# Optimization experiments

Hardware: AMD Instinct MI355X
Metric: run time of the kernel (lower is better)

Reference implementation:

```python
import jax, jax.numpy as jnp
import numpy as np

# NCHW 3x3 conv, padding=1. BatchNorm (inference affine) is folded into conv weight/bias,
# which is mathematically identical to Conv->BN(eval) in the original.
def conv3(x, w, b, stride):
    y = jax.lax.conv_general_dilated(x, w, (stride, stride), [(1, 1), (1, 1)],
                                     dimension_numbers=('NCHW', 'OIHW', 'NCHW'))
    return y + b[None, :, None, None]

def lin1(x, w, b):  # 1x1 conv as channel matmul; w: [out, in]
    return jnp.einsum('oc,bchw->bohw', w, x) + b[None, :, None, None]

def setup_inputs():
    key = jax.random.key(0)
    ks = list(jax.random.split(key, 32))
    C, M = 32, 32  # cv_hypo_num, mid_dim (kq_dim == mid_dim since mid_dim <= 128)
    B, H, W = 1, 256, 512
    w3 = lambda k, o, i: jax.random.normal(k, (o, i, 3, 3), jnp.float32) * 0.05
    w1 = lambda k, o, i: jax.random.normal(k, (o, i), jnp.float32) * 0.05
    bv = lambda k, o: jax.random.normal(k, (o,), jnp.float32) * 0.01
    inp = {
        'mono_pseudo_cost': jax.random.normal(ks[0], (B, C, H, W), jnp.float32),
        'cost_volume': jax.random.normal(ks[1], (B, C, H, W), jnp.float32),
        # mono_expand / multi_expand: two stride-2 conv(+folded BN)+ReLU blocks each
        'me_w1': w3(ks[2], M, C), 'me_b1': bv(ks[3], M),
        'me_w2': w3(ks[4], M, C), 'me_b2': bv(ks[5], M),
        'xe_w1': w3(ks[6], M, C), 'xe_b1': bv(ks[7], M),
        'xe_w2': w3(ks[8], M, C), 'xe_b2': bv(ks[9], M),
        # 1x1 q/k/v projections for both branches
        'mq_w': w1(ks[10], M, M), 'mq_b': bv(ks[11], M),
        'mk_w': w1(ks[12], M, M), 'mk_b': bv(ks[13], M),
        'mv_w': w1(ks[14], M, M), 'mv_b': bv(ks[15], M),
        'xq_w': w1(ks[16], M, M), 'xq_b': bv(ks[17], M),
        'xk_w': w1(ks[18], M, M), 'xk_b': bv(ks[19], M),
        'xv_w': w1(ks[20], M, M), 'xv_b': bv(ks[21], M),
        # residual branches
        'mr_w1': w3(ks[22], M, C), 'mr_b1': bv(ks[23], M),
        'mr_w2': w3(ks[24], M, C), 'mr_b2': bv(ks[25], M),
        'xr_w': w1(ks[26], M, C), 'xr_b': bv(ks[27], M),
        'gamma': jnp.full((1,), 0.5, jnp.float32),  # nonzero so attention path is live
    }
    return inp

def reference(mono_pseudo_cost, cost_volume,
              me_w1, me_b1, me_w2, me_b2,
              xe_w1, xe_b1, xe_w2, xe_b2,
              mq_w, mq_b, mk_w, mk_b, mv_w, mv_b,
              xq_w, xq_b, xk_w, xk_b, xv_w, xv_b,
              mr_w1, mr_b1, mr_w2, mr_b2,
              xr_w, xr_b, gamma):
    relu = jax.nn.relu
    init_h, init_w = cost_volume.shape[2], cost_volume.shape[3]
    M = me_w1.shape[0]
    # feature extractors (stride-2 x2): [B,32,256,512] -> [B,32,64,128]
    mono_feat = relu(conv3(relu(conv3(mono_pseudo_cost, me_w1, me_b1, 2)), me_w2, me_b2, 2))
    multi_feat = relu(conv3(relu(conv3(cost_volume, xe_w1, xe_b1, 2)), xe_w2, xe_b2, 2))
    b, c, h, w = multi_feat.shape
    hw = h * w
    # q/k/v as [B, C, hw]
    mono_q = lin1(mono_feat, mq_w, mq_b).reshape(b, -1, hw)
    mono_k = lin1(mono_feat, mk_w, mk_b).reshape(b, -1, hw)
    mono_v = lin1(mono_feat, mv_w, mv_b).reshape(b, -1, hw)
    multi_q = lin1(multi_feat, xq_w, xq_b).reshape(b, -1, hw)
    multi_k = lin1(multi_feat, xk_w, xk_b).reshape(b, -1, hw)
    multi_v = lin1(multi_feat, xv_w, xv_b).reshape(b, -1, hw)
    # full [B, hw, hw] attention, no 1/sqrt(d) scaling (as in original)
    mono_atten = jax.nn.softmax(jnp.einsum('bci,bcj->bij', mono_q, mono_k), axis=-1)
    multi_atten = jax.nn.softmax(jnp.einsum('bci,bcj->bij', multi_q, multi_k), axis=-1)
    # cross application: mono values weighted by multi attention and vice versa
    mono_out = jnp.einsum('bcj,bij->bci', mono_v, multi_atten).reshape(b, M, h, w)
    multi_out = jnp.einsum('bcj,bij->bci', multi_v, mono_atten).reshape(b, M, h, w)
    fused = jnp.concatenate([multi_out, mono_out], axis=1)
    # nearest-neighbor upsample back to input size (integer factor 4)
    fused = jnp.repeat(jnp.repeat(fused, init_h // h, axis=2), init_w // w, axis=3)
    # residual branches
    mono_residual = relu(conv3(relu(conv3(mono_pseudo_cost, mr_w1, mr_b1, 1)), mr_w2, mr_b2, 1))
    multi_residual = relu(lin1(cost_volume, xr_w, xr_b))
    fused = jnp.concatenate([mono_residual, multi_residual], axis=1) + gamma * fused
    return fused
```

## Files before the change

### kernel.cpp

```cpp
#include <hip/hip_runtime.h>


using bf16x8 = __attribute__((ext_vector_type(8))) short;
using f32x4  = __attribute__((ext_vector_type(4))) float;
using f32x16 = __attribute__((ext_vector_type(16))) float;
typedef unsigned short u16;
typedef unsigned int   u32;

__device__ __forceinline__ u16 f2bf(float f) {
  u32 u = __builtin_bit_cast(u32, f);
  u = (u + 0x7fffu + ((u >> 16) & 1u)) >> 16;
  return (u16)u;
}
__device__ __forceinline__ float bf2f(u16 v) {
  u32 u = ((u32)v) << 16;
  return __builtin_bit_cast(float, u);
}
__device__ __forceinline__ u32 pktr(float lo, float hi) {
  return __builtin_amdgcn_perm(__builtin_bit_cast(u32, hi),
                               __builtin_bit_cast(u32, lo), 0x07060302u);
}
__device__ __forceinline__ f32x4 mfma16(bf16x8 a, bf16x8 b, f32x4 c) {
  return __builtin_amdgcn_mfma_f32_16x16x32_bf16(a, b, c, 0, 0, 0);
}
__device__ __forceinline__ f32x16 mfma32(bf16x8 a, bf16x8 b, f32x16 c) {
  return __builtin_amdgcn_mfma_f32_32x32x16_bf16(a, b, c, 0, 0, 0);
}
__device__ __forceinline__ f32x16 zero16() {
  f32x16 z = {0,0,0,0,0,0,0,0,0,0,0,0,0,0,0,0};
  return z;
}
__device__ __forceinline__ void store4bf(u16* dst, f32x4 v) {
  u32 lo = (u32)f2bf(v[0]) | ((u32)f2bf(v[1]) << 16);
  u32 hi = (u32)f2bf(v[2]) | ((u32)f2bf(v[3]) << 16);
  *(uint2*)dst = make_uint2(lo, hi);
}
__device__ __forceinline__ float sum16(const float* e) {
  float s0 = e[0] + e[1], s1 = e[2] + e[3], s2 = e[4] + e[5], s3 = e[6] + e[7];
  float s4 = e[8] + e[9], s5 = e[10] + e[11], s6 = e[12] + e[13], s7 = e[14] + e[15];
  float a = s0 + s1, b = s2 + s3, c = s4 + s5, d = s6 + s7;
  return (a + b) + (c + d);
}

struct WPtrs { const float* p[13]; };

__global__ void k_pre(WPtrs wp, u16* __restrict__ wConv, u16* __restrict__ w1x1,
                      const float* __restrict__ mono, const float* __restrict__ cv,
                      u16* __restrict__ monoT, u16* __restrict__ cvT,
                      u16* __restrict__ m1T, u16* __restrict__ x1T, u16* __restrict__ r1T) {
  int bx = blockIdx.x, t = threadIdx.x;
  if (bx < 13) {
    if (bx < 6) {
      const float* s = wp.p[bx];
      u16* d = wConv + bx * 9216;
      for (int i = t; i < 9216; i += 256) {
        int tap = i >> 10, co = (i >> 5) & 31, ci = i & 31;
        d[i] = f2bf(s[co * 288 + ci * 9 + tap]);
      }
    } else {
      const float* s = wp.p[bx];
      u16* d = w1x1 + (bx - 6) * 1024;
      for (int i = t; i < 1024; i += 256) d[i] = f2bf(s[i]);
    }
    return;
  }
  if (bx < 138) {
    int zb = bx - 13;
    int buf = zb % 5, blk = zb / 5;
    u16* b; int Hp, Wp;
    switch (buf) {
      case 0: b = monoT; Hp = 258; Wp = 514; break;
      case 1: b = cvT;   Hp = 258; Wp = 514; break;
      case 2: b = m1T;   Hp = 130; Wp = 258; break;
      case 3: b = x1T;   Hp = 130; Wp = 258; break;
      default: b = r1T;  Hp = 258; Wp = 514; break;
    }
    int id = blk * 256 + t;
    int cell = id >> 2, c8 = (id & 3) << 3;
    if (cell >= 2 * (Hp + Wp)) return;
    int r, c;
    if (cell < Wp)              { r = 0;                 c = cell; }
    else if (cell < 2 * Wp)     { r = Hp - 1;            c = cell - Wp; }
    else if (cell < 2 * Wp + Hp){ r = cell - 2 * Wp;     c = 0; }
    else                        { r = cell - 2 * Wp - Hp; c = Wp - 1; }
    bf16x8 z = {0, 0, 0, 0, 0, 0, 0, 0};
    *(bf16x8*)&b[(r * Wp + c) * 32 + c8] = z;
    return;
  }
  int idx = bx - 138;
  int xb = idx & 7, y = (idx >> 3) & 255, z = idx >> 11;
  const float* src = z ? cv : mono;
  u16* dst = z ? cvT : monoT;
  int x0 = xb << 6;
  __shared__ u16 tile[64][40];
  int ci = t >> 3, kx = (t & 7) << 3;
  const float* sp = src + ci * 131072 + y * 512 + x0 + kx;
  float4 a = *(const float4*)sp;
  float4 bb = *(const float4*)(sp + 4);
  tile[kx + 0][ci] = f2bf(a.x); tile[kx + 1][ci] = f2bf(a.y);
  tile[kx + 2][ci] = f2bf(a.z); tile[kx + 3][ci] = f2bf(a.w);
  tile[kx + 4][ci] = f2bf(bb.x); tile[kx + 5][ci] = f2bf(bb.y);
  tile[kx + 6][ci] = f2bf(bb.z); tile[kx + 7][ci] = f2bf(bb.w);
  __syncthreads();
  int x = t >> 2, c8 = (t & 3) << 3;
  bf16x8 v = *(bf16x8*)&tile[x][c8];
  *(bf16x8*)(dst + ((y + 1) * 514 + (x0 + x + 1)) * 32 + c8) = v;
}

__device__ __forceinline__ void conv3x3_body(int bxl, int tid,
    const u16* __restrict__ inT, int Wp, const u16* __restrict__ w9,
    const float* __restrict__ bias, u16* __restrict__ out, int outPitch,
    int outOff, int Ho, int tprShift, int stride) {
  int wid = (bxl * 256 + tid) >> 6;
  int lane = tid & 63, ln = lane & 15, q = lane >> 4;
  int y = wid >> tprShift;
  int x0 = (wid & ((1 << tprShift) - 1)) << 4;
  if (y >= Ho) return;
  f32x4 acc0 = *(const f32x4*)(bias + q * 4);
  f32x4 acc1 = *(const f32x4*)(bias + 16 + q * 4);
  const u16* ib = inT + (stride * y * Wp + stride * (x0 + ln)) * 32 + q * 8;
  const u16* wb = w9 + ln * 32 + q * 8;
#pragma unroll
  for (int dy = 0; dy < 3; ++dy)
#pragma unroll
    for (int dx = 0; dx < 3; ++dx) {
      int tap = dy * 3 + dx;
      bf16x8 bf = *(const bf16x8*)(ib + (dy * Wp + dx) * 32);
      acc0 = mfma16(*(const bf16x8*)(wb + tap * 1024), bf, acc0);
      acc1 = mfma16(*(const bf16x8*)(wb + tap * 1024 + 512), bf, acc1);
    }
#pragma unroll
  for (int r = 0; r < 4; ++r) { acc0[r] = fmaxf(acc0[r], 0.f); acc1[r] = fmaxf(acc1[r], 0.f); }
  u16* ob = out + (outOff + y * outPitch + x0 + ln) * 32;
  store4bf(ob + q * 4, acc0);
  store4bf(ob + 16 + q * 4, acc1);
}

__global__ void k_convs(const u16* __restrict__ monoT, const u16* __restrict__ cvT,
                        const u16* __restrict__ wConv,
                        const float* me_b1, const float* xe_b1, const float* mr_b1,
                        u16* __restrict__ m1T, u16* __restrict__ x1T, u16* __restrict__ r1T) {
  int bx = blockIdx.x;
  if (bx < 512)
    conv3x3_body(bx, threadIdx.x, monoT, 514, wConv + 0 * 9216, me_b1, m1T, 258, 259, 128, 4, 2);
  else if (bx < 1024)
    conv3x3_body(bx - 512, threadIdx.x, cvT, 514, wConv + 2 * 9216, xe_b1, x1T, 258, 259, 128, 4, 2);
  else
    conv3x3_body(bx - 1024, threadIdx.x, monoT, 514, wConv + 4 * 9216, mr_b1, r1T, 514, 515, 256, 5, 1);
}

__global__ void k_feat(const u16* __restrict__ m1T, const u16* __restrict__ x1T,
                       const u16* __restrict__ wConv,
                       const float* me_b2, const float* xe_b2,
                       u16* __restrict__ featM, u16* __restrict__ featX) {
  int bx = blockIdx.x;
  if (bx < 128)
    conv3x3_body(bx, threadIdx.x, m1T, 258, wConv + 1 * 9216, me_b2, featM, 128, 0, 64, 3, 2);
  else
    conv3x3_body(bx - 128, threadIdx.x, x1T, 258, wConv + 3 * 9216, xe_b2, featX, 128, 0, 64, 3, 2);
}

__global__ void k_proj(const u16* __restrict__ featM, const u16* __restrict__ featX,
                       const u16* __restrict__ w1x1,
                       const float* mq_b, const float* mk_b, const float* mv_b,
                       const float* xq_b, const float* xk_b, const float* xv_b,
                       u16* Qm, u16* Km, u16* Vm, u16* Qx, u16* Kx, u16* Vx) {
  int which = blockIdx.y;
  const u16* feat = (which < 3) ? featM : featX;
  const float* bias; u16* dst; float scale = 1.f; int cmode = 0;
  switch (which) {
    case 0: bias = mq_b; dst = Qm; scale = 1.4426950408889634f; break;
    case 1: bias = mk_b; dst = Km; break;
    case 2: bias = mv_b; dst = Vm; cmode = 1; break;
    case 3: bias = xq_b; dst = Qx; scale = 1.4426950408889634f; break;
    case 4: bias = xk_b; dst = Kx; break;
    default: bias = xv_b; dst = Vx; cmode = 1; break;
  }
  const u16* w = w1x1 + which * 1024;
  int wave = threadIdx.x >> 6, lane = threadIdx.x & 63, ln = lane & 15, q = lane >> 4;
  int p0 = (blockIdx.x * 4 + wave) << 4;
  bf16x8 bf = *(const bf16x8*)(feat + (p0 + ln) * 32 + q * 8);
  bf16x8 a0 = *(const bf16x8*)(w + ln * 32 + q * 8);
  bf16x8 a1 = *(const bf16x8*)(w + (16 + ln) * 32 + q * 8);
  f32x4 acc0 = *(const f32x4*)(bias + q * 4);
  f32x4 acc1 = *(const f32x4*)(bias + 16 + q * 4);
  acc0 = mfma16(a0, bf, acc0);
  acc1 = mfma16(a1, bf, acc1);
#pragma unroll
  for (int r = 0; r < 4; ++r) { acc0[r] *= scale; acc1[r] *= scale; }
  if (!cmode) {
    store4bf(dst + (p0 + ln) * 32 + q * 4, acc0);
    store4bf(dst + (p0 + ln) * 32 + 16 + q * 4, acc1);
  } else {
    int p = p0 + ln;
    int jl = p & 63, jb = p & ~63;
    int pj = jb + (jl >> 5) * 32 + ((jl >> 4) & 1) * 16 + ((jl >> 2) & 1) * 8
           + ((jl >> 3) & 1) * 4 + (jl & 3);
#pragma unroll
    for (int r = 0; r < 4; ++r) {
      dst[(q * 4 + r) * 8192 + pj] = f2bf(acc0[r]);
      dst[(16 + q * 4 + r) * 8192 + pj] = f2bf(acc1[r]);
    }
  }
}

__global__ void __launch_bounds__(256, 4) k_attention(
    const u16* __restrict__ Qm, const u16* __restrict__ Km, const u16* __restrict__ Vm,
    const u16* __restrict__ Qx, const u16* __restrict__ Kx, const u16* __restrict__ Vx,
    u16* __restrict__ Opart, float* __restrict__ lpart) {
  const u16 *Qp, *Kp, *Vp;
  int att = blockIdx.z;
  if (att == 0) { Qp = Qm; Kp = Km; Vp = Vx; }
  else          { Qp = Qx; Kp = Kx; Vp = Vm; }
  int sp = blockIdx.y;
  int j0 = sp << 10;

  __shared__ u16 Kl[2][64][40];
  __shared__ u16 Vl[2][32][72];

  int t = threadIdx.x, wave = t >> 6, lane = t & 63, ln = lane & 31, h = lane >> 5;
  int iw = blockIdx.x * 128 + wave * 32;

  bf16x8 qf0 = *(const bf16x8*)(Qp + (iw + ln) * 32 + h * 8);
  bf16x8 qf1 = *(const bf16x8*)(Qp + (iw + ln) * 32 + 16 + h * 8);

  int krow = t >> 2, kcol = (t & 3) << 3;
  int vrow = t >> 3, vcol = (t & 7) << 3;
  const u16* Kg = Kp + j0 * 32;
  const u16* Vg = Vp + j0;

  bf16x8 kn = *(const bf16x8*)(Kg + t * 8);
  bf16x8 vn = *(const bf16x8*)(Vg + vrow * 8192 + vcol);
  *(bf16x8*)&Kl[0][krow][kcol] = kn;
  *(bf16x8*)&Vl[0][vrow][vcol] = vn;

  f32x16 O = zero16();
  float lsum = 0.f;

  for (int jt = 0; jt < 16; ++jt) {
    __syncthreads();
    bool have = (jt + 1) < 16;
    if (have) {
      kn = *(const bf16x8*)(Kg + (jt + 1) * 2048 + t * 8);
      vn = *(const bf16x8*)(Vg + vrow * 8192 + (jt + 1) * 64 + vcol);
    }
    int cur = jt & 1;
#pragma unroll
    for (int hh = 0; hh < 2; ++hh) {
      f32x16 s = mfma32(*(const bf16x8*)&Kl[cur][hh * 32 + ln][h * 8], qf0, zero16());
      s = mfma32(*(const bf16x8*)&Kl[cur][hh * 32 + ln][16 + h * 8], qf1, s);
      float e[16];
#pragma unroll
      for (int r = 0; r < 16; ++r) e[r] = __builtin_amdgcn_exp2f(s[r]);
      lsum += sum16(e);
      union PF { bf16x8 v; u32 w[4]; } pf0, pf1;
#pragma unroll
      for (int p = 0; p < 4; ++p) {
        pf0.w[p] = pktr(e[2 * p], e[2 * p + 1]);
        pf1.w[p] = pktr(e[8 + 2 * p], e[8 + 2 * p + 1]);
      }
      bf16x8 vf0 = *(const bf16x8*)&Vl[cur][ln][(2 * hh) * 16 + h * 8];
      bf16x8 vf1 = *(const bf16x8*)&Vl[cur][ln][(2 * hh + 1) * 16 + h * 8];
      O = mfma32(pf0.v, vf0, O);
      O = mfma32(pf1.v, vf1, O);
    }
    if (have) {
      *(bf16x8*)&Kl[1 - cur][krow][kcol] = kn;
      *(bf16x8*)&Vl[1 - cur][vrow][vcol] = vn;
    }
  }
  u16* ob = Opart + (size_t)(att * 8 + sp) * 262144;
  float* lb = lpart + (att * 8 + sp) * 8192;
#pragma unroll
  for (int r = 0; r < 16; ++r) {
    int ig = iw + (r & 3) + 8 * (r >> 2) + 4 * h;
    ob[ig * 32 + ln] = f2bf(O[r]);
  }
  float lo = __shfl(lsum, lane ^ 32, 64);
  float lt = lsum + lo;
  if (lane < 32) lb[iw + lane] = lt;
}

__global__ void k_reduce(const u16* __restrict__ Opart, const float* __restrict__ lpart,
                         float* __restrict__ attA, float* __restrict__ attB) {
  int a = blockIdx.y;
  int id = blockIdx.x * 256 + threadIdx.x;
  int i = id >> 5, c = id & 31;
  float s = 0.f, l = 0.f;
#pragma unroll
  for (int sp = 0; sp < 8; ++sp) {
    s += bf2f(Opart[(size_t)(a * 8 + sp) * 262144 + id]);
    l += lpart[(a * 8 + sp) * 8192 + i];
  }
  float* out = a ? attB : attA;
  out[i * 32 + c] = s / l;
}

__global__ void k_final(const u16* __restrict__ r1T, const u16* __restrict__ cvT,
                        const u16* __restrict__ wConv, const u16* __restrict__ w1x1,
                        const float* mr_b2, const float* xr_b,
                        const float* __restrict__ attA, const float* __restrict__ attB,
                        const float* __restrict__ gamma, float* __restrict__ dout) {
  int bx = blockIdx.x, tid = threadIdx.x;
  int lane = tid & 63, ln = lane & 15, q = lane >> 4;
  float g = gamma[0];
  if (bx < 2048) {
    const u16* w9 = wConv + 5 * 9216;
    int wid = (bx * 256 + tid) >> 6;
    int y = wid >> 5, x0 = (wid & 31) << 4;
    f32x4 acc0 = *(const f32x4*)(mr_b2 + q * 4);
    f32x4 acc1 = *(const f32x4*)(mr_b2 + 16 + q * 4);
    const u16* ib = r1T + (y * 514 + x0 + ln) * 32 + q * 8;
    const u16* wb = w9 + ln * 32 + q * 8;
#pragma unroll
    for (int dy = 0; dy < 3; ++dy)
#pragma unroll
      for (int dx = 0; dx < 3; ++dx) {
        int tap = dy * 3 + dx;
        bf16x8 bf = *(const bf16x8*)(ib + (dy * 514 + dx) * 32);
        acc0 = mfma16(*(const bf16x8*)(wb + tap * 1024), bf, acc0);
        acc1 = mfma16(*(const bf16x8*)(wb + tap * 1024 + 512), bf, acc1);
      }
    int xg = x0 + ln;
    const float* ap = attA + ((y >> 2) * 128 + (xg >> 2)) * 32;
    float* ob = dout + y * 512 + xg;
#pragma unroll
    for (int r = 0; r < 4; ++r) {
      int co0 = q * 4 + r, co1 = 16 + q * 4 + r;
      ob[co0 * 131072] = fmaxf(acc0[r], 0.f) + g * ap[co0];
      ob[co1 * 131072] = fmaxf(acc1[r], 0.f) + g * ap[co1];
    }
  } else {
    const u16* w = w1x1 + 6 * 1024;
    int wid = ((bx - 2048) * 256 + tid) >> 6;
    int p0 = wid << 4;
    int y = p0 >> 9, x0 = p0 & 511;
    bf16x8 bf = *(const bf16x8*)(cvT + ((y + 1) * 514 + x0 + ln + 1) * 32 + q * 8);
    f32x4 acc0 = *(const f32x4*)(xr_b + q * 4);
    f32x4 acc1 = *(const f32x4*)(xr_b + 16 + q * 4);
    acc0 = mfma16(*(const bf16x8*)(w + ln * 32 + q * 8), bf, acc0);
    acc1 = mfma16(*(const bf16x8*)(w + (16 + ln) * 32 + q * 8), bf, acc1);
    int xg = x0 + ln;
    const float* ap = attB + ((y >> 2) * 128 + (xg >> 2)) * 32;
    float* ob = dout + 32 * 131072 + p0 + ln;
#pragma unroll
    for (int r = 0; r < 4; ++r) {
      int co0 = q * 4 + r, co1 = 16 + q * 4 + r;
      ob[co0 * 131072] = fmaxf(acc0[r], 0.f) + g * ap[co0];
      ob[co1 * 131072] = fmaxf(acc1[r], 0.f) + g * ap[co1];
    }
  }
}

extern "C" void kernel_launch(void* const* d_in, const int* in_sizes, int n_in,
                              void* d_out, int out_size, void* d_ws, size_t ws_size,
                              hipStream_t stream) {
  const float* mono  = (const float*)d_in[0];
  const float* cv    = (const float*)d_in[1];
  const float* me_b1 = (const float*)d_in[3];
  const float* me_b2 = (const float*)d_in[5];
  const float* xe_b1 = (const float*)d_in[7];
  const float* xe_b2 = (const float*)d_in[9];
  const float* mq_b  = (const float*)d_in[11];
  const float* mk_b  = (const float*)d_in[13];
  const float* mv_b  = (const float*)d_in[15];
  const float* xq_b  = (const float*)d_in[17];
  const float* xk_b  = (const float*)d_in[19];
  const float* xv_b  = (const float*)d_in[21];
  const float* mr_b2 = (const float*)d_in[25];
  const float* mr_b1 = (const float*)d_in[23];
  const float* xr_b  = (const float*)d_in[27];
  const float* gamma = (const float*)d_in[28];
  float* dout = (float*)d_out;

  char* ws = (char*)d_ws;
  u16* wConv = (u16*)(ws + 0);
  u16* w1x1  = (u16*)(ws + 110592);
  u16* monoT = (u16*)(ws + 124928);
  u16* Opart = (u16*)(ws + 124928);
  u16* cvT   = (u16*)(ws + 8612096);
  u16* m1T   = (u16*)(ws + 17099264);
  u16* x1T   = (u16*)(ws + 19245824);
  u16* r1T   = (u16*)(ws + 21392384);
  u16* featM = (u16*)(ws + 29879552);
  u16* featX = (u16*)(ws + 30403840);
  u16* Qm    = (u16*)(ws + 30928128);
  u16* Km    = (u16*)(ws + 31452416);
  u16* Vm    = (u16*)(ws + 31976704);
  u16* Qx    = (u16*)(ws + 32500992);
  u16* Kx    = (u16*)(ws + 33025280);
  u16* Vx    = (u16*)(ws + 33549568);
  float* attA  = (float*)(ws + 34073856);
  float* attB  = (float*)(ws + 35122432);
  float* lpart = (float*)(ws + 36171008);

  WPtrs wp;
  wp.p[0] = (const float*)d_in[2];
  wp.p[1] = (const float*)d_in[4];
  wp.p[2] = (const float*)d_in[6];
  wp.p[3] = (const float*)d_in[8];
  wp.p[4] = (const float*)d_in[22];
  wp.p[5] = (const float*)d_in[24];
  wp.p[6] = (const float*)d_in[10];
  wp.p[7] = (const float*)d_in[12];
  wp.p[8] = (const float*)d_in[14];
  wp.p[9] = (const float*)d_in[16];
  wp.p[10] = (const float*)d_in[18];
  wp.p[11] = (const float*)d_in[20];
  wp.p[12] = (const float*)d_in[26];

  k_pre<<<4234, 256, 0, stream>>>(wp, wConv, w1x1, mono, cv, monoT, cvT, m1T, x1T, r1T);
  k_convs<<<3072, 256, 0, stream>>>(monoT, cvT, wConv, me_b1, xe_b1, mr_b1, m1T, x1T, r1T);
  k_feat<<<256, 256, 0, stream>>>(m1T, x1T, wConv, me_b2, xe_b2, featM, featX);
  k_proj<<<dim3(128, 6), 256, 0, stream>>>(featM, featX, w1x1,
                                           mq_b, mk_b, mv_b, xq_b, xk_b, xv_b,
                                           Qm, Km, Vm, Qx, Kx, Vx);
  k_attention<<<dim3(64, 8, 2), 256, 0, stream>>>(Qm, Km, Vm, Qx, Kx, Vx, Opart, lpart);
  k_reduce<<<dim3(1024, 2), 256, 0, stream>>>(Opart, lpart, attA, attB);
  k_final<<<4096, 256, 0, stream>>>(r1T, cvT, wConv, w1x1, mr_b2, xr_b, attA, attB, gamma, dout);
}
```

Measured before the change: 218.6 us.

## Fuse feature conv with QKV projection and fold attention reduce into final kernel

Merges the second stride-2 conv and the 1x1 q/k/v projections into one kernel that stages the feature tile in shared memory. This removes the featM/featX round trip and one launch. The split-K attention reduction (summing partial outputs and normalising by l) now runs inside the final output kernel, which drops the separate reduce kernel and the attA/attB buffers. The cost is that each output pixel re-reads 8 partial slices for its attention pixel, 16 times over because of the 4x4 upsample, so k_final does more redundant global reads.

```diff
diff --git a/kernel.cpp b/kernel.cpp
--- a/kernel.cpp
+++ b/kernel.cpp
@@ -16,6 +16,8 @@
   u32 u = ((u32)v) << 16;
   return __builtin_bit_cast(float, u);
 }
+__device__ __forceinline__ float bfLO(u32 u) { return __builtin_bit_cast(float, u << 16); }
+__device__ __forceinline__ float bfHI(u32 u) { return __builtin_bit_cast(float, u & 0xffff0000u); }
 __device__ __forceinline__ u32 pktr(float lo, float hi) {
   return __builtin_amdgcn_perm(__builtin_bit_cast(u32, hi),
                                __builtin_bit_cast(u32, lo), 0x07060302u);
@@ -149,57 +151,75 @@
     conv3x3_body(bx - 1024, threadIdx.x, monoT, 514, wConv + 4 * 9216, mr_b1, r1T, 514, 515, 256, 5, 1);
 }
 
-__global__ void k_feat(const u16* __restrict__ m1T, const u16* __restrict__ x1T,
-                       const u16* __restrict__ wConv,
-                       const float* me_b2, const float* xe_b2,
-                       u16* __restrict__ featM, u16* __restrict__ featX) {
-  int bx = blockIdx.x;
-  if (bx < 128)
-    conv3x3_body(bx, threadIdx.x, m1T, 258, wConv + 1 * 9216, me_b2, featM, 128, 0, 64, 3, 2);
-  else
-    conv3x3_body(bx - 128, threadIdx.x, x1T, 258, wConv + 3 * 9216, xe_b2, featX, 128, 0, 64, 3, 2);
-}
-
-__global__ void k_proj(const u16* __restrict__ featM, const u16* __restrict__ featX,
-                       const u16* __restrict__ w1x1,
-                       const float* mq_b, const float* mk_b, const float* mv_b,
-                       const float* xq_b, const float* xk_b, const float* xv_b,
-                       u16* Qm, u16* Km, u16* Vm, u16* Qx, u16* Kx, u16* Vx) {
-  int which = blockIdx.y;
-  const u16* feat = (which < 3) ? featM : featX;
-  const float* bias; u16* dst; float scale = 1.f; int cmode = 0;
-  switch (which) {
-    case 0: bias = mq_b; dst = Qm; scale = 1.4426950408889634f; break;
-    case 1: bias = mk_b; dst = Km; break;
-    case 2: bias = mv_b; dst = Vm; cmode = 1; break;
-    case 3: bias = xq_b; dst = Qx; scale = 1.4426950408889634f; break;
-    case 4: bias = xk_b; dst = Kx; break;
-    default: bias = xv_b; dst = Vx; cmode = 1; break;
-  }
-  const u16* w = w1x1 + which * 1024;
-  int wave = threadIdx.x >> 6, lane = threadIdx.x & 63, ln = lane & 15, q = lane >> 4;
-  int p0 = (blockIdx.x * 4 + wave) << 4;
-  bf16x8 bf = *(const bf16x8*)(feat + (p0 + ln) * 32 + q * 8);
-  bf16x8 a0 = *(const bf16x8*)(w + ln * 32 + q * 8);
-  bf16x8 a1 = *(const bf16x8*)(w + (16 + ln) * 32 + q * 8);
-  f32x4 acc0 = *(const f32x4*)(bias + q * 4);
-  f32x4 acc1 = *(const f32x4*)(bias + 16 + q * 4);
-  acc0 = mfma16(a0, bf, acc0);
-  acc1 = mfma16(a1, bf, acc1);
-#pragma unroll
-  for (int r = 0; r < 4; ++r) { acc0[r] *= scale; acc1[r] *= scale; }
-  if (!cmode) {
-    store4bf(dst + (p0 + ln) * 32 + q * 4, acc0);
-    store4bf(dst + (p0 + ln) * 32 + 16 + q * 4, acc1);
-  } else {
-    int p = p0 + ln;
-    int jl = p & 63, jb = p & ~63;
-    int pj = jb + (jl >> 5) * 32 + ((jl >> 4) & 1) * 16 + ((jl >> 2) & 1) * 8
-           + ((jl >> 3) & 1) * 4 + (jl & 3);
-#pragma unroll
-    for (int r = 0; r < 4; ++r) {
-      dst[(q * 4 + r) * 8192 + pj] = f2bf(acc0[r]);
-      dst[(16 + q * 4 + r) * 8192 + pj] = f2bf(acc1[r]);
+__global__ void k_featproj(const u16* __restrict__ m1T, const u16* __restrict__ x1T,
+                           const u16* __restrict__ wConv, const u16* __restrict__ w1x1,
+                           const float* me_b2, const float* xe_b2,
+                           const float* mq_b, const float* mk_b, const float* mv_b,
+                           const float* xq_b, const float* xk_b, const float* xv_b,
+                           u16* Qm, u16* Km, u16* Vm, u16* Qx, u16* Kx, u16* Vx) {
+  int bx = blockIdx.x, br = blockIdx.y;
+  const u16* inT = br ? x1T : m1T;
+  const u16* w9 = wConv + (br ? 3 : 1) * 9216;
+  const float* bias2 = br ? xe_b2 : me_b2;
+  __shared__ u16 fs[64][40];
+  int tid = threadIdx.x, wave = tid >> 6, lane = tid & 63, ln = lane & 15, q = lane >> 4;
+  int fy = bx >> 1, x0 = (bx & 1) * 64 + wave * 16;
+  {
+    f32x4 acc0 = *(const f32x4*)(bias2 + q * 4);
+    f32x4 acc1 = *(const f32x4*)(bias2 + 16 + q * 4);
+    const u16* ib = inT + (2 * fy * 258 + 2 * (x0 + ln)) * 32 + q * 8;
+    const u16* wb = w9 + ln * 32 + q * 8;
+#pragma unroll
+    for (int dy = 0; dy < 3; ++dy)
+#pragma unroll
+      for (int dx = 0; dx < 3; ++dx) {
+        int tap = dy * 3 + dx;
+        bf16x8 bf = *(const bf16x8*)(ib + (dy * 258 + dx) * 32);
+        acc0 = mfma16(*(const bf16x8*)(wb + tap * 1024), bf, acc0);
+        acc1 = mfma16(*(const bf16x8*)(wb + tap * 1024 + 512), bf, acc1);
+      }
+#pragma unroll
+    for (int r = 0; r < 4; ++r) { acc0[r] = fmaxf(acc0[r], 0.f); acc1[r] = fmaxf(acc1[r], 0.f); }
+    int row = wave * 16 + ln;
+    store4bf(&fs[row][q * 4], acc0);
+    store4bf(&fs[row][16 + q * 4], acc1);
+  }
+  __syncthreads();
+  int p = fy * 128 + x0 + ln;
+  bf16x8 bf = *(const bf16x8*)&fs[wave * 16 + ln][q * 8];
+#pragma unroll
+  for (int wh = 0; wh < 3; ++wh) {
+    int which = br * 3 + wh;
+    const float* bias; u16* dst; float scale = 1.f; int cmode = 0;
+    switch (which) {
+      case 0: bias = mq_b; dst = Qm; scale = 1.4426950408889634f; break;
+      case 1: bias = mk_b; dst = Km; break;
+      case 2: bias = mv_b; dst = Vm; cmode = 1; break;
+      case 3: bias = xq_b; dst = Qx; scale = 1.4426950408889634f; break;
+      case 4: bias = xk_b; dst = Kx; break;
+      default: bias = xv_b; dst = Vx; cmode = 1; break;
+    }
+    const u16* w = w1x1 + which * 1024;
+    bf16x8 a0 = *(const bf16x8*)(w + ln * 32 + q * 8);
+    bf16x8 a1 = *(const bf16x8*)(w + (16 + ln) * 32 + q * 8);
+    f32x4 acc0 = *(const f32x4*)(bias + q * 4);
+    f32x4 acc1 = *(const f32x4*)(bias + 16 + q * 4);
+    acc0 = mfma16(a0, bf, acc0);
+    acc1 = mfma16(a1, bf, acc1);
+#pragma unroll
+    for (int r = 0; r < 4; ++r) { acc0[r] *= scale; acc1[r] *= scale; }
+    if (!cmode) {
+      store4bf(dst + p * 32 + q * 4, acc0);
+      store4bf(dst + p * 32 + 16 + q * 4, acc1);
+    } else {
+      int jl = p & 63, jb = p & ~63;
+      int pj = jb + (jl >> 5) * 32 + ((jl >> 4) & 1) * 16 + ((jl >> 2) & 1) * 8
+             + ((jl >> 3) & 1) * 4 + (jl & 3);
+#pragma unroll
+      for (int r = 0; r < 4; ++r) {
+        dst[(q * 4 + r) * 8192 + pj] = f2bf(acc0[r]);
+        dst[(16 + q * 4 + r) * 8192 + pj] = f2bf(acc1[r]);
+      }
     }
   }
 }
@@ -281,25 +301,30 @@
   if (lane < 32) lb[iw + lane] = lt;
 }
 
-__global__ void k_reduce(const u16* __restrict__ Opart, const float* __restrict__ lpart,
-                         float* __restrict__ attA, float* __restrict__ attB) {
-  int a = blockIdx.y;
-  int id = blockIdx.x * 256 + threadIdx.x;
-  int i = id >> 5, c = id & 31;
-  float s = 0.f, l = 0.f;
+__device__ __forceinline__ void att_reduce(const u16* __restrict__ Opart,
+                                           const float* __restrict__ lpart,
+                                           int a, int apix, int q, float g,
+                                           f32x4& vA, f32x4& vB) {
+  f32x4 sA = {0, 0, 0, 0}, sB = {0, 0, 0, 0};
+  float l = 0.f;
 #pragma unroll
   for (int sp = 0; sp < 8; ++sp) {
-    s += bf2f(Opart[(size_t)(a * 8 + sp) * 262144 + id]);
-    l += lpart[(a * 8 + sp) * 8192 + i];
-  }
-  float* out = a ? attB : attA;
-  out[i * 32 + c] = s / l;
+    const u16* op = Opart + (size_t)(a * 8 + sp) * 262144 + apix * 32;
+    uint2 w0 = *(const uint2*)(op + q * 4);
+    uint2 w1 = *(const uint2*)(op + 16 + q * 4);
+    sA[0] += bfLO(w0.x); sA[1] += bfHI(w0.x); sA[2] += bfLO(w0.y); sA[3] += bfHI(w0.y);
+    sB[0] += bfLO(w1.x); sB[1] += bfHI(w1.x); sB[2] += bfLO(w1.y); sB[3] += bfHI(w1.y);
+    l += lpart[(a * 8 + sp) * 8192 + apix];
+  }
+  float gl = g / l;
+#pragma unroll
+  for (int r = 0; r < 4; ++r) { vA[r] = sA[r] * gl; vB[r] = sB[r] * gl; }
 }
 
 __global__ void k_final(const u16* __restrict__ r1T, const u16* __restrict__ cvT,
                         const u16* __restrict__ wConv, const u16* __restrict__ w1x1,
                         const float* mr_b2, const float* xr_b,
-                        const float* __restrict__ attA, const float* __restrict__ attB,
+                        const u16* __restrict__ Opart, const float* __restrict__ lpart,
                         const float* __restrict__ gamma, float* __restrict__ dout) {
   int bx = blockIdx.x, tid = threadIdx.x;
   int lane = tid & 63, ln = lane & 15, q = lane >> 4;
@@ -322,13 +347,15 @@
         acc1 = mfma16(*(const bf16x8*)(wb + tap * 1024 + 512), bf, acc1);
       }
     int xg = x0 + ln;
-    const float* ap = attA + ((y >> 2) * 128 + (xg >> 2)) * 32;
+    int apix = (y >> 2) * 128 + (xg >> 2);
+    f32x4 vA, vB;
+    att_reduce(Opart, lpart, 0, apix, q, g, vA, vB);
     float* ob = dout + y * 512 + xg;
 #pragma unroll
     for (int r = 0; r < 4; ++r) {
       int co0 = q * 4 + r, co1 = 16 + q * 4 + r;
-      ob[co0 * 131072] = fmaxf(acc0[r], 0.f) + g * ap[co0];
-      ob[co1 * 131072] = fmaxf(acc1[r], 0.f) + g * ap[co1];
+      ob[co0 * 131072] = fmaxf(acc0[r], 0.f) + vA[r];
+      ob[co1 * 131072] = fmaxf(acc1[r], 0.f) + vB[r];
     }
   } else {
     const u16* w = w1x1 + 6 * 1024;
@@ -341,13 +368,15 @@
     acc0 = mfma16(*(const bf16x8*)(w + ln * 32 + q * 8), bf, acc0);
     acc1 = mfma16(*(const bf16x8*)(w + (16 + ln) * 32 + q * 8), bf, acc1);
     int xg = x0 + ln;
-    const float* ap = attB + ((y >> 2) * 128 + (xg >> 2)) * 32;
+    int apix = (y >> 2) * 128 + (xg >> 2);
+    f32x4 vA, vB;
+    att_reduce(Opart, lpart, 1, apix, q, g, vA, vB);
     float* ob = dout + 32 * 131072 + p0 + ln;
 #pragma unroll
     for (int r = 0; r < 4; ++r) {
       int co0 = q * 4 + r, co1 = 16 + q * 4 + r;
-      ob[co0 * 131072] = fmaxf(acc0[r], 0.f) + g * ap[co0];
-      ob[co1 * 131072] = fmaxf(acc1[r], 0.f) + g * ap[co1];
+      ob[co0 * 131072] = fmaxf(acc0[r], 0.f) + vA[r];
+      ob[co1 * 131072] = fmaxf(acc1[r], 0.f) + vB[r];
     }
   }
 }
@@ -367,8 +396,8 @@
   const float* xq_b  = (const float*)d_in[17];
   const float* xk_b  = (const float*)d_in[19];
   const float* xv_b  = (const float*)d_in[21];
+  const float* mr_b1 = (const float*)d_in[23];
   const float* mr_b2 = (const float*)d_in[25];
-  const float* mr_b1 = (const float*)d_in[23];
   const float* xr_b  = (const float*)d_in[27];
   const float* gamma = (const float*)d_in[28];
   float* dout = (float*)d_out;
@@ -382,16 +411,12 @@
   u16* m1T   = (u16*)(ws + 17099264);
   u16* x1T   = (u16*)(ws + 19245824);
   u16* r1T   = (u16*)(ws + 21392384);
-  u16* featM = (u16*)(ws + 29879552);
-  u16* featX = (u16*)(ws + 30403840);
   u16* Qm    = (u16*)(ws + 30928128);
   u16* Km    = (u16*)(ws + 31452416);
   u16* Vm    = (u16*)(ws + 31976704);
   u16* Qx    = (u16*)(ws + 32500992);
   u16* Kx    = (u16*)(ws + 33025280);
   u16* Vx    = (u16*)(ws + 33549568);
-  float* attA  = (float*)(ws + 34073856);
-  float* attB  = (float*)(ws + 35122432);
   float* lpart = (float*)(ws + 36171008);
 
   WPtrs wp;
@@ -411,11 +436,9 @@
 
   k_pre<<<4234, 256, 0, stream>>>(wp, wConv, w1x1, mono, cv, monoT, cvT, m1T, x1T, r1T);
   k_convs<<<3072, 256, 0, stream>>>(monoT, cvT, wConv, me_b1, xe_b1, mr_b1, m1T, x1T, r1T);
-  k_feat<<<256, 256, 0, stream>>>(m1T, x1T, wConv, me_b2, xe_b2, featM, featX);
-  k_proj<<<dim3(128, 6), 256, 0, stream>>>(featM, featX, w1x1,
-                                           mq_b, mk_b, mv_b, xq_b, xk_b, xv_b,
-                                           Qm, Km, Vm, Qx, Kx, Vx);
+  k_featproj<<<dim3(128, 2), 256, 0, stream>>>(m1T, x1T, wConv, w1x1, me_b2, xe_b2,
+                                               mq_b, mk_b, mv_b, xq_b, xk_b, xv_b,
+                                               Qm, Km, Vm, Qx, Kx, Vx);
   k_attention<<<dim3(64, 8, 2), 256, 0, stream>>>(Qm, Km, Vm, Qx, Kx, Vx, Opart, lpart);
-  k_reduce<<<dim3(1024, 2), 256, 0, stream>>>(Opart, lpart, attA, attB);
-  k_final<<<4096, 256, 0, stream>>>(r1T, cvT, wConv, w1x1, mr_b2, xr_b, attA, attB, gamma, dout);
-}
+  k_final<<<4096, 256, 0, stream>>>(r1T, cvT, wConv, w1x1, mr_b2, xr_b, Opart, lpart, gamma, dout);
+}
```

Result: no change. 214.6 us (-1.9%).
